# Kernel optimization log

Hardware: AMD Instinct MI355X
Metric: run time of the kernel (lower is better)

The kernel has to match this reference:

```python
import jax, jax.numpy as jnp
import numpy as np

IN_CH = 256
LATENT = 32

def setup_inputs() -> dict:
    key = jax.random.key(0)
    k1, k2, k3 = jax.random.split(key, 3)
    x = jax.random.normal(k1, (8, IN_CH, 64, 64), dtype=jnp.float32)
    # 1x1 conv weights stored as [out, in] matrices
    w_qk = jax.random.normal(k2, (2 * LATENT, IN_CH), dtype=jnp.float32) * (IN_CH ** -0.5)
    w_v = jax.random.normal(k3, (IN_CH, IN_CH), dtype=jnp.float32) * (IN_CH ** -0.5)
    gamma = jnp.zeros((1,), dtype=jnp.float32) + 0.5  # nonzero so attention path matters
    return {"x": x, "w_qk": w_qk, "w_v": w_v, "gamma": gamma}

def reference(x, w_qk, w_v, gamma):
    b, c, h, w = x.shape
    xf = x.reshape(b, c, h * w)                      # [b, c, s]
    qk = jnp.einsum('oc,bcs->bos', w_qk, xf)          # 1x1 conv == matmul
    q, k = qk[:, :LATENT], qk[:, LATENT:]             # [b, L, s] each
    v = jnp.einsum('oc,bcs->bos', w_v, xf)            # [b, c, s]
    scale = 1.0 / LATENT ** 0.25
    m = jnp.einsum('bcs,bct->bst', scale * q, scale * k)  # [b, s, s]
    m = jax.nn.softmax(m, axis=-1)
    a = jnp.einsum('bst,bct->bcs', m, v)              # [b, c, s]
    a = a.reshape(b, c, h, w)
    return gamma * a + x
```

## Files before the change

kernel.cpp:

```cpp
#include <hip/hip_runtime.h>

typedef __attribute__((ext_vector_type(4)))  float f32x4;
typedef __attribute__((ext_vector_type(16))) float f32x16;
typedef __attribute__((ext_vector_type(8)))  short short8;
typedef __attribute__((ext_vector_type(4)))  unsigned short u16x4;
typedef __attribute__((ext_vector_type(4)))  unsigned int u32x4;
typedef __attribute__((ext_vector_type(2)))  unsigned int u32x2;

static __device__ __forceinline__ unsigned short f2bf(float f) {
    unsigned int u = __float_as_uint(f);
    unsigned int r = (u + 0x7FFFu + ((u >> 16) & 1u)) >> 16;
    return (unsigned short)r;
}

#if __has_builtin(__builtin_amdgcn_exp2f)
#define EXP2(x) __builtin_amdgcn_exp2f(x)
#else
#define EXP2(x) exp2f(x)
#endif

static __device__ __forceinline__ u32x2 swap32v(unsigned int a, unsigned int b) {
#if __has_builtin(__builtin_amdgcn_permlane32_swap)
    return __builtin_amdgcn_permlane32_swap(a, b, false, false);
#else
    asm("v_permlane32_swap_b32 %0, %1" : "+v"(a), "+v"(b));
    u32x2 r; r[0] = a; r[1] = b; return r;
#endif
}

static __device__ __forceinline__ void block_sync_lds() {
    asm volatile("s_waitcnt lgkmcnt(0)" ::: "memory");
    __builtin_amdgcn_s_barrier();
    asm volatile("" ::: "memory");
}

#define SCALE2Q 0.25503487756f

__global__ void prep_w_kernel(const float* __restrict__ wqk,
                              const float* __restrict__ wv,
                              unsigned short* __restrict__ W) {
    int idx = blockIdx.x * 256 + threadIdx.x;
    int o = idx >> 8, c = idx & 255;
    float v;
    if (o < 64) { v = wqk[o * 256 + c]; if (o < 32) v *= SCALE2Q; }
    else        { v = wv[(o - 64) * 256 + c]; }
    W[idx] = f2bf(v);
}

__global__ __launch_bounds__(256) void transpose_kernel(
        const float* __restrict__ x, unsigned short* __restrict__ xT) {
    __shared__ unsigned short tile[64][66];
    int b = blockIdx.x & 7;
    int rem = blockIdx.x >> 3;
    int ct = rem >> 6, st = rem & 63;
    int s0 = st * 64, c0 = ct * 64;
    int tid = threadIdx.x;
    int ss = tid & 63, cq = tid >> 6;
#pragma unroll
    for (int p = 0; p < 16; ++p) {
        int cc = p * 4 + cq;
        float v = x[(size_t)(b * 256 + c0 + cc) * 4096 + s0 + ss];
        tile[ss][cc] = f2bf(v);
    }
    __syncthreads();
#pragma unroll
    for (int p = 0; p < 8; ++p) {
        int idx = p * 256 + tid;
        int sr = idx >> 5, jj = idx & 31;
        unsigned int val = *(const unsigned int*)&tile[sr][jj * 2];
        *(unsigned int*)(xT + (size_t)(b * 4096 + s0 + sr) * 256 + c0 + jj * 2) = val;
    }
}

__global__ __launch_bounds__(256) void proj_kernel(
        const unsigned short* __restrict__ W,
        const unsigned short* __restrict__ xT,
        unsigned short* __restrict__ qkT,
        unsigned short* __restrict__ vbuf) {
    const int b  = blockIdx.x & 7;
    const int sb = blockIdx.x >> 3;
    const int s0 = sb * 64;
    const int tid = threadIdx.x;
    const int w = tid >> 6, l = tid & 63;
    const int lg = l >> 4, ll = l & 15;
    const size_t xbase = (size_t)b * 4096 * 256;

    f32x4 acc[5][4];
#pragma unroll
    for (int ot = 0; ot < 5; ++ot)
#pragma unroll
        for (int st = 0; st < 4; ++st) acc[ot][st] = (f32x4)0.0f;

    for (int k0 = 0; k0 < 256; k0 += 32) {
        short8 bf[4], af[5];
#pragma unroll
        for (int st = 0; st < 4; ++st)
            bf[st] = *(const short8*)(xT + xbase + (size_t)(s0 + st * 16 + ll) * 256 + k0 + lg * 8);
#pragma unroll
        for (int ot = 0; ot < 5; ++ot)
            af[ot] = *(const short8*)(W + (size_t)(80 * w + ot * 16 + ll) * 256 + k0 + lg * 8);
#pragma unroll
        for (int ot = 0; ot < 5; ++ot)
#pragma unroll
            for (int st = 0; st < 4; ++st)
                acc[ot][st] = __builtin_amdgcn_mfma_f32_16x16x32_bf16(af[ot], bf[st], acc[ot][st], 0, 0, 0);
    }
#pragma unroll
    for (int ot = 0; ot < 5; ++ot) {
        int o0 = 80 * w + ot * 16 + lg * 4;
#pragma unroll
        for (int st = 0; st < 4; ++st) {
            int s = s0 + st * 16 + ll;
            if (o0 < 64) {
                u16x4 pk;
#pragma unroll
                for (int i = 0; i < 4; ++i) pk[i] = f2bf(acc[ot][st][i]);
                *(u16x4*)(qkT + (size_t)b * 4096 * 64 + (size_t)s * 64 + o0) = pk;
            } else {
#pragma unroll
                for (int i = 0; i < 4; ++i)
                    vbuf[(size_t)b * 256 * 4096 + (size_t)(o0 - 64 + i) * 4096 + s] = f2bf(acc[ot][st][i]);
            }
        }
    }
}

__global__ __launch_bounds__(256) void repack_v_kernel(
        const unsigned short* __restrict__ vbuf,
        unsigned short* __restrict__ vfrag) {
    int idx = blockIdx.x * 256 + threadIdx.x;
    int l    = idx & 63;
    int kf16 = (idx >> 6) & 255;
    int ct4  = (idx >> 14) & 7;
    int b    = idx >> 17;
    int l31 = l & 31, l5 = l >> 5;
    short8 v = *(const short8*)(vbuf + (size_t)b * 256 * 4096
                                + (size_t)(32 * ct4 + l31) * 4096
                                + 16 * kf16 + 8 * l5);
    *(short8*)(vfrag + (size_t)idx * 8) = v;
}

__global__ __launch_bounds__(256) void repack_k_kernel(
        const unsigned short* __restrict__ qkT,
        unsigned short* __restrict__ kfrag) {
    int idx = blockIdx.x * 256 + threadIdx.x;
    int l  = idx & 63;
    int h  = (idx >> 6) & 1;
    int t2 = (idx >> 7) & 127;
    int b  = idx >> 14;
    int l31 = l & 31, l5 = l >> 5;
    short8 v = *(const short8*)(qkT + (size_t)b * 4096 * 64
                                + (size_t)(32 * t2 + l31) * 64
                                + 32 + 16 * h + 8 * l5);
    *(short8*)(kfrag + (size_t)idx * 8) = v;
}

__global__ __launch_bounds__(512, 2) void attn_kernel(
        const unsigned short* __restrict__ qkT,
        const unsigned short* __restrict__ kfrag,
        const unsigned short* __restrict__ vfrag,
        const float* __restrict__ x,
        const float* __restrict__ gamma,
        float* __restrict__ out) {
    __shared__ unsigned short p_lds[2][4][4][64][8];
    __shared__ float lsum_lds[128];

    const int b   = blockIdx.x & 7;
    const int sb  = blockIdx.x >> 3;
    const int s0  = sb * 128;
    const int w   = threadIdx.x >> 6;
    const int l   = threadIdx.x & 63;
    const int l5  = l >> 5, l31 = l & 31;

    const size_t qk_base = (size_t)b * 4096 * 64;
    const size_t bx_base = (size_t)b * 256 * 4096;

    if (w < 4) {
        const unsigned short* qrow = qkT + qk_base + (size_t)(s0 + 32 * w + l31) * 64;
        const short8 qf0 = *(const short8*)(qrow + 8 * l5);
        const short8 qf1 = *(const short8*)(qrow + 16 + 8 * l5);
        const unsigned short* kfp = kfrag + (size_t)b * 128 * 2 * 512 + 8 * l;
        const f32x16 z16 = (f32x16)0.0f;
        float psum = 0.f;

        short8 kf00 = *(const short8*)(kfp + 0 * 512);
        short8 kf01 = *(const short8*)(kfp + 1 * 512);
        short8 kf10 = *(const short8*)(kfp + 2 * 512);
        short8 kf11 = *(const short8*)(kfp + 3 * 512);

#define EXPPACK(DD, PLO, PHI)                                                  \
    {                                                                          \
        float e0 = EXP2((DD)[0]),   e1 = EXP2((DD)[1]);                        \
        float e2 = EXP2((DD)[2]),   e3 = EXP2((DD)[3]);                        \
        float e4 = EXP2((DD)[4]),   e5 = EXP2((DD)[5]);                        \
        float e6 = EXP2((DD)[6]),   e7 = EXP2((DD)[7]);                        \
        float e8 = EXP2((DD)[8]),   e9 = EXP2((DD)[9]);                        \
        float e10 = EXP2((DD)[10]), e11 = EXP2((DD)[11]);                      \
        float e12 = EXP2((DD)[12]), e13 = EXP2((DD)[13]);                      \
        float e14 = EXP2((DD)[14]), e15 = EXP2((DD)[15]);                      \
        psum += (((e0 + e1) + (e2 + e3)) + ((e4 + e5) + (e6 + e7)))            \
              + (((e8 + e9) + (e10 + e11)) + ((e12 + e13) + (e14 + e15)));     \
        unsigned int c0, c1, c2, c3;                                           \
        asm("v_cvt_pk_bf16_f32 %0, %1, %2" : "=v"(c0) : "v"(e0), "v"(e1));     \
        asm("v_cvt_pk_bf16_f32 %0, %1, %2" : "=v"(c1) : "v"(e2), "v"(e3));     \
        asm("v_cvt_pk_bf16_f32 %0, %1, %2" : "=v"(c2) : "v"(e4), "v"(e5));     \
        asm("v_cvt_pk_bf16_f32 %0, %1, %2" : "=v"(c3) : "v"(e6), "v"(e7));     \
        u32x2 s0_ = swap32v(c0, c2);                                           \
        u32x2 s1_ = swap32v(c1, c3);                                           \
        u32x4 lo_; lo_[0] = s0_[0]; lo_[1] = s1_[0]; lo_[2] = s0_[1]; lo_[3] = s1_[1]; \
        PLO = __builtin_bit_cast(short8, lo_);                                 \
        unsigned int d0, d1, d2, d3;                                           \
        asm("v_cvt_pk_bf16_f32 %0, %1, %2" : "=v"(d0) : "v"(e8), "v"(e9));     \
        asm("v_cvt_pk_bf16_f32 %0, %1, %2" : "=v"(d1) : "v"(e10), "v"(e11));   \
        asm("v_cvt_pk_bf16_f32 %0, %1, %2" : "=v"(d2) : "v"(e12), "v"(e13));   \
        u32x2 s2_ = swap32v(d0, d2);                                           \
        asm("v_cvt_pk_bf16_f32 %0, %1, %2" : "=v"(d3) : "v"(e14), "v"(e15));   \
        u32x2 s3_ = swap32v(d1, d3);                                           \
        u32x4 hi_; hi_[0] = s2_[0]; hi_[1] = s3_[0]; hi_[2] = s2_[1]; hi_[3] = s3_[1]; \
        PHI = __builtin_bit_cast(short8, hi_);                                 \
    }

#define PRODUCE(T)                                                             \
    {                                                                          \
        const int tn_ = ((T) + 1) & 63;                                        \
        const int pb_ = (T) & 1;                                               \
        f32x16 dd0 = __builtin_amdgcn_mfma_f32_32x32x16_bf16(kf00, qf0, z16, 0, 0, 0); \
        dd0 = __builtin_amdgcn_mfma_f32_32x32x16_bf16(kf01, qf1, dd0, 0, 0, 0);\
        f32x16 dd1 = __builtin_amdgcn_mfma_f32_32x32x16_bf16(kf10, qf0, z16, 0, 0, 0); \
        dd1 = __builtin_amdgcn_mfma_f32_32x32x16_bf16(kf11, qf1, dd1, 0, 0, 0);\
        kf00 = *(const short8*)(kfp + (size_t)(4 * tn_ + 0) * 512);            \
        kf01 = *(const short8*)(kfp + (size_t)(4 * tn_ + 1) * 512);            \
        kf10 = *(const short8*)(kfp + (size_t)(4 * tn_ + 2) * 512);            \
        kf11 = *(const short8*)(kfp + (size_t)(4 * tn_ + 3) * 512);            \
        short8 pa0, pa1, pa2, pa3;                                             \
        EXPPACK(dd0, pa0, pa1)                                                 \
        EXPPACK(dd1, pa2, pa3)                                                 \
        *(short8*)&p_lds[pb_][w][0][l][0] = pa0;                               \
        *(short8*)&p_lds[pb_][w][1][l][0] = pa1;                               \
        *(short8*)&p_lds[pb_][w][2][l][0] = pa2;                               \
        *(short8*)&p_lds[pb_][w][3][l][0] = pa3;                               \
    }

        PRODUCE(0)
        for (int t = 1; t < 64; ++t) {
            block_sync_lds();
            PRODUCE(t)
        }
        block_sync_lds();
#undef PRODUCE
#undef EXPPACK

        psum += __shfl_xor(psum, 32);
        if (l5 == 0) lsum_lds[32 * w + l31] = psum;
        __syncthreads();
    } else {
        const int cw = w - 4;
        const int ct0 = 2 * cw, ct1 = 2 * cw + 1;
        const unsigned short* vfp0 = vfrag + ((size_t)(b * 8 + ct0) * 256) * 512 + 8 * l;
        const unsigned short* vfp1 = vfrag + ((size_t)(b * 8 + ct1) * 256) * 512 + 8 * l;

        f32x16 a00 = (f32x16)0.0f, a10 = (f32x16)0.0f;
        f32x16 a20 = (f32x16)0.0f, a30 = (f32x16)0.0f;
        f32x16 a01 = (f32x16)0.0f, a11 = (f32x16)0.0f;
        f32x16 a21 = (f32x16)0.0f, a31 = (f32x16)0.0f;
        short8 vA0 = *(const short8*)(vfp0 + 0 * 512);
        short8 vA1 = *(const short8*)(vfp1 + 0 * 512);
        short8 vB0 = *(const short8*)(vfp0 + 1 * 512);
        short8 vB1 = *(const short8*)(vfp1 + 1 * 512);

#define CKS(KS, V0, V1)                                                        \
        {                                                                      \
            short8 p0 = *(const short8*)&p_lds[pb][0][KS][l][0];               \
            short8 p1 = *(const short8*)&p_lds[pb][1][KS][l][0];               \
            short8 p2 = *(const short8*)&p_lds[pb][2][KS][l][0];               \
            short8 p3 = *(const short8*)&p_lds[pb][3][KS][l][0];               \
            a00 = __builtin_amdgcn_mfma_f32_32x32x16_bf16(p0, V0, a00, 0, 0, 0); \
            a10 = __builtin_amdgcn_mfma_f32_32x32x16_bf16(p1, V0, a10, 0, 0, 0); \
            a20 = __builtin_amdgcn_mfma_f32_32x32x16_bf16(p2, V0, a20, 0, 0, 0); \
            a30 = __builtin_amdgcn_mfma_f32_32x32x16_bf16(p3, V0, a30, 0, 0, 0); \
            a01 = __builtin_amdgcn_mfma_f32_32x32x16_bf16(p0, V1, a01, 0, 0, 0); \
            a11 = __builtin_amdgcn_mfma_f32_32x32x16_bf16(p1, V1, a11, 0, 0, 0); \
            a21 = __builtin_amdgcn_mfma_f32_32x32x16_bf16(p2, V1, a21, 0, 0, 0); \
            a31 = __builtin_amdgcn_mfma_f32_32x32x16_bf16(p3, V1, a31, 0, 0, 0); \
        }

        for (int t = 0; t < 64; ++t) {
            block_sync_lds();
            const int pb = t & 1;
            const int tn = (t + 1) & 63;
            CKS(0, vA0, vA1)
            vA0 = *(const short8*)(vfp0 + (size_t)(4 * t + 2) * 512);
            vA1 = *(const short8*)(vfp1 + (size_t)(4 * t + 2) * 512);
            CKS(1, vB0, vB1)
            vB0 = *(const short8*)(vfp0 + (size_t)(4 * t + 3) * 512);
            vB1 = *(const short8*)(vfp1 + (size_t)(4 * t + 3) * 512);
            CKS(2, vA0, vA1)
            vA0 = *(const short8*)(vfp0 + (size_t)(4 * tn + 0) * 512);
            vA1 = *(const short8*)(vfp1 + (size_t)(4 * tn + 0) * 512);
            CKS(3, vB0, vB1)
            vB0 = *(const short8*)(vfp0 + (size_t)(4 * tn + 1) * 512);
            vB1 = *(const short8*)(vfp1 + (size_t)(4 * tn + 1) * 512);
        }
#undef CKS
        __syncthreads();

        const float g = gamma[0];
#pragma unroll
        for (int rq = 0; rq < 4; ++rq) {
            const int rbase = 8 * rq + 4 * l5;
#define STORE_QB(ACC, QB, CT)                                                  \
            {                                                                  \
                f32x4 ls = *(const f32x4*)&lsum_lds[32 * (QB) + rbase];        \
                f32x4 gi;                                                      \
                gi[0] = g / ls[0]; gi[1] = g / ls[1];                          \
                gi[2] = g / ls[2]; gi[3] = g / ls[3];                          \
                size_t off = bx_base + (size_t)(32 * (CT) + l31) * 4096 + s0 + 32 * (QB) + rbase; \
                f32x4 xv = *(const f32x4*)(x + off);                           \
                f32x4 o;                                                       \
                o[0] = gi[0] * (ACC)[4 * rq + 0] + xv[0];                      \
                o[1] = gi[1] * (ACC)[4 * rq + 1] + xv[1];                      \
                o[2] = gi[2] * (ACC)[4 * rq + 2] + xv[2];                      \
                o[3] = gi[3] * (ACC)[4 * rq + 3] + xv[3];                      \
                *(f32x4*)(out + off) = o;                                      \
            }
            STORE_QB(a00, 0, ct0)
            STORE_QB(a10, 1, ct0)
            STORE_QB(a20, 2, ct0)
            STORE_QB(a30, 3, ct0)
            STORE_QB(a01, 0, ct1)
            STORE_QB(a11, 1, ct1)
            STORE_QB(a21, 2, ct1)
            STORE_QB(a31, 3, ct1)
#undef STORE_QB
        }
    }
}

extern "C" void kernel_launch(void* const* d_in, const int* in_sizes, int n_in,
                              void* d_out, int out_size, void* d_ws, size_t ws_size,
                              hipStream_t stream) {
    const float* x     = (const float*)d_in[0];
    const float* wqk   = (const float*)d_in[1];
    const float* wv    = (const float*)d_in[2];
    const float* gamma = (const float*)d_in[3];
    float* out = (float*)d_out;

    char* ws = (char*)d_ws;
    unsigned short* W     = (unsigned short*)(ws);
    unsigned short* qkT   = (unsigned short*)(ws + 163840);
    unsigned short* xT    = (unsigned short*)(ws + 4358144);
    unsigned short* vbuf  = (unsigned short*)(ws + 21135360);
    unsigned short* kfrag = (unsigned short*)(ws + 37912576);
    unsigned short* vfrag = xT;

    hipLaunchKernelGGL(prep_w_kernel,    dim3(320),  dim3(256), 0, stream, wqk, wv, W);
    hipLaunchKernelGGL(transpose_kernel, dim3(2048), dim3(256), 0, stream, x, xT);
    hipLaunchKernelGGL(proj_kernel,      dim3(512),  dim3(256), 0, stream, W, xT, qkT, vbuf);
    hipLaunchKernelGGL(repack_v_kernel,  dim3(4096), dim3(256), 0, stream, vbuf, vfrag);
    hipLaunchKernelGGL(repack_k_kernel,  dim3(512),  dim3(256), 0, stream, qkT, kfrag);
    hipLaunchKernelGGL(attn_kernel,      dim3(256),  dim3(512), 0, stream, qkT, kfrag, vfrag, x, gamma, out);
}
```

Measured before the change: 143.8 us.

## Fuse V repack into projection and shrink attention tile to 64 queries

The projection kernel now writes V directly in MFMA fragment layout through an LDS staging tile, so the separate repack_v kernel and its full round trip through global memory are removed. The attention kernel handles 64 query rows per block with 2 softmax waves and 4 PV waves (384 threads, 3 blocks per CU), which doubles the grid to 512 blocks for better CU fill. K and V fragments are now re-read by twice as many blocks. s_setprio hints are also added around the MFMA groups.

```diff
diff --git a/kernel.cpp b/kernel.cpp
--- a/kernel.cpp
+++ b/kernel.cpp
@@ -76,7 +76,8 @@
         const unsigned short* __restrict__ W,
         const unsigned short* __restrict__ xT,
         unsigned short* __restrict__ qkT,
-        unsigned short* __restrict__ vbuf) {
+        unsigned short* __restrict__ vfrag) {
+    __shared__ unsigned short vtile[8][4][64][8];
     const int b  = blockIdx.x & 7;
     const int sb = blockIdx.x >> 3;
     const int s0 = sb * 64;
@@ -110,34 +111,29 @@
         int o0 = 80 * w + ot * 16 + lg * 4;
 #pragma unroll
         for (int st = 0; st < 4; ++st) {
-            int s = s0 + st * 16 + ll;
+            int sl = st * 16 + ll;
             if (o0 < 64) {
                 u16x4 pk;
 #pragma unroll
                 for (int i = 0; i < 4; ++i) pk[i] = f2bf(acc[ot][st][i]);
-                *(u16x4*)(qkT + (size_t)b * 4096 * 64 + (size_t)s * 64 + o0) = pk;
+                *(u16x4*)(qkT + (size_t)b * 4096 * 64 + (size_t)(s0 + sl) * 64 + o0) = pk;
             } else {
 #pragma unroll
-                for (int i = 0; i < 4; ++i)
-                    vbuf[(size_t)b * 256 * 4096 + (size_t)(o0 - 64 + i) * 4096 + s] = f2bf(acc[ot][st][i]);
+                for (int i = 0; i < 4; ++i) {
+                    int c = o0 - 64 + i;
+                    vtile[c >> 5][sl >> 4][(c & 31) + 32 * ((sl >> 3) & 1)][sl & 7]
+                        = f2bf(acc[ot][st][i]);
+                }
             }
         }
     }
-}
-
-__global__ __launch_bounds__(256) void repack_v_kernel(
-        const unsigned short* __restrict__ vbuf,
-        unsigned short* __restrict__ vfrag) {
-    int idx = blockIdx.x * 256 + threadIdx.x;
-    int l    = idx & 63;
-    int kf16 = (idx >> 6) & 255;
-    int ct4  = (idx >> 14) & 7;
-    int b    = idx >> 17;
-    int l31 = l & 31, l5 = l >> 5;
-    short8 v = *(const short8*)(vbuf + (size_t)b * 256 * 4096
-                                + (size_t)(32 * ct4 + l31) * 4096
-                                + 16 * kf16 + 8 * l5);
-    *(short8*)(vfrag + (size_t)idx * 8) = v;
+    __syncthreads();
+    const int wv = w;
+#pragma unroll
+    for (int ct4 = 0; ct4 < 8; ++ct4) {
+        short8 v = *(const short8*)&vtile[ct4][wv][l][0];
+        *(short8*)(vfrag + ((size_t)((b * 8 + ct4) * 256) + sb * 4 + wv) * 512 + 8 * l) = v;
+    }
 }
 
 __global__ __launch_bounds__(256) void repack_k_kernel(
@@ -155,19 +151,19 @@
     *(short8*)(kfrag + (size_t)idx * 8) = v;
 }
 
-__global__ __launch_bounds__(512, 2) void attn_kernel(
+__global__ __launch_bounds__(384, 3) void attn_kernel(
         const unsigned short* __restrict__ qkT,
         const unsigned short* __restrict__ kfrag,
         const unsigned short* __restrict__ vfrag,
         const float* __restrict__ x,
         const float* __restrict__ gamma,
         float* __restrict__ out) {
-    __shared__ unsigned short p_lds[2][4][4][64][8];
-    __shared__ float lsum_lds[128];
+    __shared__ unsigned short p_lds[2][2][4][64][8];
+    __shared__ float lsum_lds[64];
 
     const int b   = blockIdx.x & 7;
     const int sb  = blockIdx.x >> 3;
-    const int s0  = sb * 128;
+    const int s0  = sb * 64;
     const int w   = threadIdx.x >> 6;
     const int l   = threadIdx.x & 63;
     const int l5  = l >> 5, l31 = l & 31;
@@ -175,7 +171,7 @@
     const size_t qk_base = (size_t)b * 4096 * 64;
     const size_t bx_base = (size_t)b * 256 * 4096;
 
-    if (w < 4) {
+    if (w < 2) {
         const unsigned short* qrow = qkT + qk_base + (size_t)(s0 + 32 * w + l31) * 64;
         const short8 qf0 = *(const short8*)(qrow + 8 * l5);
         const short8 qf1 = *(const short8*)(qrow + 16 + 8 * l5);
@@ -224,10 +220,12 @@
     {                                                                          \
         const int tn_ = ((T) + 1) & 63;                                        \
         const int pb_ = (T) & 1;                                               \
+        __builtin_amdgcn_s_setprio(1);                                         \
         f32x16 dd0 = __builtin_amdgcn_mfma_f32_32x32x16_bf16(kf00, qf0, z16, 0, 0, 0); \
         dd0 = __builtin_amdgcn_mfma_f32_32x32x16_bf16(kf01, qf1, dd0, 0, 0, 0);\
         f32x16 dd1 = __builtin_amdgcn_mfma_f32_32x32x16_bf16(kf10, qf0, z16, 0, 0, 0); \
         dd1 = __builtin_amdgcn_mfma_f32_32x32x16_bf16(kf11, qf1, dd1, 0, 0, 0);\
+        __builtin_amdgcn_s_setprio(0);                                         \
         kf00 = *(const short8*)(kfp + (size_t)(4 * tn_ + 0) * 512);            \
         kf01 = *(const short8*)(kfp + (size_t)(4 * tn_ + 1) * 512);            \
         kf10 = *(const short8*)(kfp + (size_t)(4 * tn_ + 2) * 512);            \
@@ -254,50 +252,50 @@
         if (l5 == 0) lsum_lds[32 * w + l31] = psum;
         __syncthreads();
     } else {
-        const int cw = w - 4;
+        const int cw = w - 2;
         const int ct0 = 2 * cw, ct1 = 2 * cw + 1;
         const unsigned short* vfp0 = vfrag + ((size_t)(b * 8 + ct0) * 256) * 512 + 8 * l;
         const unsigned short* vfp1 = vfrag + ((size_t)(b * 8 + ct1) * 256) * 512 + 8 * l;
 
         f32x16 a00 = (f32x16)0.0f, a10 = (f32x16)0.0f;
-        f32x16 a20 = (f32x16)0.0f, a30 = (f32x16)0.0f;
         f32x16 a01 = (f32x16)0.0f, a11 = (f32x16)0.0f;
-        f32x16 a21 = (f32x16)0.0f, a31 = (f32x16)0.0f;
         short8 vA0 = *(const short8*)(vfp0 + 0 * 512);
         short8 vA1 = *(const short8*)(vfp1 + 0 * 512);
         short8 vB0 = *(const short8*)(vfp0 + 1 * 512);
         short8 vB1 = *(const short8*)(vfp1 + 1 * 512);
 
-#define CKS(KS, V0, V1)                                                        \
+#define CKS(PB, KS, V0, V1)                                                    \
         {                                                                      \
-            short8 p0 = *(const short8*)&p_lds[pb][0][KS][l][0];               \
-            short8 p1 = *(const short8*)&p_lds[pb][1][KS][l][0];               \
-            short8 p2 = *(const short8*)&p_lds[pb][2][KS][l][0];               \
-            short8 p3 = *(const short8*)&p_lds[pb][3][KS][l][0];               \
+            short8 p0 = *(const short8*)&p_lds[PB][0][KS][l][0];               \
+            short8 p1 = *(const short8*)&p_lds[PB][1][KS][l][0];               \
             a00 = __builtin_amdgcn_mfma_f32_32x32x16_bf16(p0, V0, a00, 0, 0, 0); \
             a10 = __builtin_amdgcn_mfma_f32_32x32x16_bf16(p1, V0, a10, 0, 0, 0); \
-            a20 = __builtin_amdgcn_mfma_f32_32x32x16_bf16(p2, V0, a20, 0, 0, 0); \
-            a30 = __builtin_amdgcn_mfma_f32_32x32x16_bf16(p3, V0, a30, 0, 0, 0); \
             a01 = __builtin_amdgcn_mfma_f32_32x32x16_bf16(p0, V1, a01, 0, 0, 0); \
             a11 = __builtin_amdgcn_mfma_f32_32x32x16_bf16(p1, V1, a11, 0, 0, 0); \
-            a21 = __builtin_amdgcn_mfma_f32_32x32x16_bf16(p2, V1, a21, 0, 0, 0); \
-            a31 = __builtin_amdgcn_mfma_f32_32x32x16_bf16(p3, V1, a31, 0, 0, 0); \
         }
 
         for (int t = 0; t < 64; ++t) {
             block_sync_lds();
             const int pb = t & 1;
             const int tn = (t + 1) & 63;
-            CKS(0, vA0, vA1)
+            __builtin_amdgcn_s_setprio(1);
+            CKS(pb, 0, vA0, vA1)
+            __builtin_amdgcn_s_setprio(0);
             vA0 = *(const short8*)(vfp0 + (size_t)(4 * t + 2) * 512);
             vA1 = *(const short8*)(vfp1 + (size_t)(4 * t + 2) * 512);
-            CKS(1, vB0, vB1)
+            __builtin_amdgcn_s_setprio(1);
+            CKS(pb, 1, vB0, vB1)
+            __builtin_amdgcn_s_setprio(0);
             vB0 = *(const short8*)(vfp0 + (size_t)(4 * t + 3) * 512);
             vB1 = *(const short8*)(vfp1 + (size_t)(4 * t + 3) * 512);
-            CKS(2, vA0, vA1)
+            __builtin_amdgcn_s_setprio(1);
+            CKS(pb, 2, vA0, vA1)
+            __builtin_amdgcn_s_setprio(0);
             vA0 = *(const short8*)(vfp0 + (size_t)(4 * tn + 0) * 512);
             vA1 = *(const short8*)(vfp1 + (size_t)(4 * tn + 0) * 512);
-            CKS(3, vB0, vB1)
+            __builtin_amdgcn_s_setprio(1);
+            CKS(pb, 3, vB0, vB1)
+            __builtin_amdgcn_s_setprio(0);
             vB0 = *(const short8*)(vfp0 + (size_t)(4 * tn + 1) * 512);
             vB1 = *(const short8*)(vfp1 + (size_t)(4 * tn + 1) * 512);
         }
@@ -325,12 +323,8 @@
             }
             STORE_QB(a00, 0, ct0)
             STORE_QB(a10, 1, ct0)
-            STORE_QB(a20, 2, ct0)
-            STORE_QB(a30, 3, ct0)
             STORE_QB(a01, 0, ct1)
             STORE_QB(a11, 1, ct1)
-            STORE_QB(a21, 2, ct1)
-            STORE_QB(a31, 3, ct1)
 #undef STORE_QB
         }
     }
@@ -349,14 +343,12 @@
     unsigned short* W     = (unsigned short*)(ws);
     unsigned short* qkT   = (unsigned short*)(ws + 163840);
     unsigned short* xT    = (unsigned short*)(ws + 4358144);
-    unsigned short* vbuf  = (unsigned short*)(ws + 21135360);
+    unsigned short* vfrag = (unsigned short*)(ws + 21135360);
     unsigned short* kfrag = (unsigned short*)(ws + 37912576);
-    unsigned short* vfrag = xT;
 
     hipLaunchKernelGGL(prep_w_kernel,    dim3(320),  dim3(256), 0, stream, wqk, wv, W);
     hipLaunchKernelGGL(transpose_kernel, dim3(2048), dim3(256), 0, stream, x, xT);
-    hipLaunchKernelGGL(proj_kernel,      dim3(512),  dim3(256), 0, stream, W, xT, qkT, vbuf);
-    hipLaunchKernelGGL(repack_v_kernel,  dim3(4096), dim3(256), 0, stream, vbuf, vfrag);
+    hipLaunchKernelGGL(proj_kernel,      dim3(512),  dim3(256), 0, stream, W, xT, qkT, vfrag);
     hipLaunchKernelGGL(repack_k_kernel,  dim3(512),  dim3(256), 0, stream, qkT, kfrag);
-    hipLaunchKernelGGL(attn_kernel,      dim3(256),  dim3(512), 0, stream, qkT, kfrag, vfrag, x, gamma, out);
-}
+    hipLaunchKernelGGL(attn_kernel,      dim3(512),  dim3(384), 0, stream, qkT, kfrag, vfrag, x, gamma, out);
+}
```

Measured after the change: 128.6 us. 10.6% less time.
